# Optimization experiments

Measured on AMD Instinct MI355X. Metric: run time of the kernel, lower is better.

## Reference

```python
import jax, jax.numpy as jnp
import numpy as np

DIM = 1024
DIM_HEADS = 64  # number of heads in this module (per-head dim is 1, see source quirk)


def setup_inputs() -> dict:
    key = jax.random.key(0)
    k1, k2, k3 = jax.random.split(key, 3)
    x = jax.random.normal(k1, (1, 2048, DIM), dtype=jnp.float32)
    # torch Linear weight layout: [out_features, in_features]
    w_qkv = jax.random.normal(k2, (DIM_HEADS * 3, DIM), dtype=jnp.float32) * 0.02
    w_out = jax.random.normal(k3, (DIM, DIM_HEADS), dtype=jnp.float32) * 0.02
    return {"x": x, "w_qkv": w_qkv, "w_out": w_out}


def reference(x, w_qkv, w_out):
    b, n, _ = x.shape
    h = DIM_HEADS
    qkv = jnp.einsum('bnc,fc->bnf', x, w_qkv)          # [b, n, 3*h]
    q, k, v = jnp.split(qkv, 3, axis=-1)                # each [b, n, h]
    # rearrange 'b n (h d) -> b h n d' with h = DIM_HEADS => d = 1
    q = q.transpose(0, 2, 1)[..., None]                 # [b, h, n, 1]
    k = k.transpose(0, 2, 1)[..., None]
    v = v.transpose(0, 2, 1)[..., None]
    scale = 1.0 / jnp.sqrt(jnp.float32(h))              # source divides by sqrt(dim_heads)
    dots = jnp.einsum('bhid,bhjd->bhij', q, k) * scale  # [b, h, n, n]
    causal = jnp.tril(jnp.ones((n, n), dtype=bool))
    dots = jnp.where(causal, dots, -jnp.inf)
    attn = jax.nn.softmax(dots, axis=-1)
    out = jnp.einsum('bhij,bhjd->bhid', attn, v)        # [b, h, n, 1]
    out = out[..., 0].transpose(0, 2, 1)                # [b, n, h]
    return jnp.einsum('bnh,ch->bnc', out, w_out)        # [b, n, dim]
```

## Files before the change

kernel.cpp:

```cpp
#include <hip/hip_runtime.h>


#if __has_builtin(__builtin_amdgcn_exp2f)
#define EXP2F(x) __builtin_amdgcn_exp2f(x)
#else
#define EXP2F(x) exp2f(x)
#endif

#define LOG2E_DIV8 0.18033688011112042f

__global__ __launch_bounds__(256) void prep_kernel(const float* __restrict__ wqkv,
                                                   const float* __restrict__ wout,
                                                   float* __restrict__ wT,
                                                   float* __restrict__ wOutT) {
    const int b = blockIdx.x;
    if (b < 768) {
        int idx = b * 256 + threadIdx.x;
        int f = idx >> 10, k = idx & 1023;
        float val = wqkv[idx];
        if (f >= 64 && f < 128) val *= LOG2E_DIV8;
        wT[k * 192 + f] = val;
    } else {
        int idx = (b - 768) * 256 + threadIdx.x;
        int cc = idx >> 6, hh = idx & 63;
        wOutT[hh * 1024 + cc] = wout[idx];
    }
}

__global__ __launch_bounds__(256) void qkv_gemm(const float* __restrict__ x,
                                                const float* __restrict__ wT,
                                                float* __restrict__ pq) {
    __shared__ float xsT[32][64];
    __shared__ float wsld[32][64];
    const int t = threadIdx.x;
    const int b = blockIdx.x;
    const int ks = b & 7;
    const int nt = (b >> 3) % 3;
    const int mt = b / 24;
    const int i0 = mt * 64;
    const int cb = nt * 64;
    const int k0 = ks * 128;

    const int rf = t & 63;
    const int kq = t >> 6;
    const int tx = t & 15;
    const int ty = t >> 4;

    const float* xp = x + (size_t)(i0 + rf) * 1024 + k0 + kq * 8;
    const float* wp = wT + (size_t)(k0 + kq * 8) * 192 + cb + rf;

    float4 xa = *(const float4*)(xp);
    float4 xb = *(const float4*)(xp + 4);
    float wr[8];
#pragma unroll
    for (int j = 0; j < 8; ++j) wr[j] = wp[(size_t)j * 192];

    float acc[4][4] = {};

    for (int s = 0; s < 4; ++s) {
        __syncthreads();
        {
            const int kb = kq * 8;
            xsT[kb + 0][rf] = xa.x; xsT[kb + 1][rf] = xa.y;
            xsT[kb + 2][rf] = xa.z; xsT[kb + 3][rf] = xa.w;
            xsT[kb + 4][rf] = xb.x; xsT[kb + 5][rf] = xb.y;
            xsT[kb + 6][rf] = xb.z; xsT[kb + 7][rf] = xb.w;
#pragma unroll
            for (int j = 0; j < 8; ++j) wsld[kb + j][rf] = wr[j];
        }
        __syncthreads();
        if (s < 3) {
            const float* xp2 = xp + (s + 1) * 32;
            xa = *(const float4*)(xp2);
            xb = *(const float4*)(xp2 + 4);
            const float* wp2 = wp + (size_t)(s + 1) * 32 * 192;
#pragma unroll
            for (int j = 0; j < 8; ++j) wr[j] = wp2[(size_t)j * 192];
        }
#pragma unroll
        for (int k = 0; k < 32; ++k) {
            float4 a4 = *(const float4*)&xsT[k][ty * 4];
            float4 b4 = *(const float4*)&wsld[k][tx * 4];
            acc[0][0] = fmaf(a4.x, b4.x, acc[0][0]);
            acc[0][1] = fmaf(a4.x, b4.y, acc[0][1]);
            acc[0][2] = fmaf(a4.x, b4.z, acc[0][2]);
            acc[0][3] = fmaf(a4.x, b4.w, acc[0][3]);
            acc[1][0] = fmaf(a4.y, b4.x, acc[1][0]);
            acc[1][1] = fmaf(a4.y, b4.y, acc[1][1]);
            acc[1][2] = fmaf(a4.y, b4.z, acc[1][2]);
            acc[1][3] = fmaf(a4.y, b4.w, acc[1][3]);
            acc[2][0] = fmaf(a4.z, b4.x, acc[2][0]);
            acc[2][1] = fmaf(a4.z, b4.y, acc[2][1]);
            acc[2][2] = fmaf(a4.z, b4.z, acc[2][2]);
            acc[2][3] = fmaf(a4.z, b4.w, acc[2][3]);
            acc[3][0] = fmaf(a4.w, b4.x, acc[3][0]);
            acc[3][1] = fmaf(a4.w, b4.y, acc[3][1]);
            acc[3][2] = fmaf(a4.w, b4.z, acc[3][2]);
            acc[3][3] = fmaf(a4.w, b4.w, acc[3][3]);
        }
    }

    float* pbase = pq + (size_t)ks * 192 * 2048 + (size_t)cb * 2048 + i0;
#pragma unroll
    for (int cc = 0; cc < 4; ++cc) {
        float4 o = make_float4(acc[0][cc], acc[1][cc], acc[2][cc], acc[3][cc]);
        *(float4*)(pbase + (size_t)(tx * 4 + cc) * 2048 + ty * 4) = o;
    }
}

__global__ __launch_bounds__(256) void qkv_reduce(const float* __restrict__ pq,
                                                  float* __restrict__ qsv) {
    const int idx = blockIdx.x * 256 + threadIdx.x;
    const int f = idx >> 9;
    const int i = (idx & 511) * 4;
    const size_t S = (size_t)192 * 2048;
    const size_t o = (size_t)f * 2048 + i;
    float4 a0 = *(const float4*)(pq + o);
    float4 a1 = *(const float4*)(pq + S + o);
    float4 a2 = *(const float4*)(pq + 2 * S + o);
    float4 a3 = *(const float4*)(pq + 3 * S + o);
    float4 a4 = *(const float4*)(pq + 4 * S + o);
    float4 a5 = *(const float4*)(pq + 5 * S + o);
    float4 a6 = *(const float4*)(pq + 6 * S + o);
    float4 a7 = *(const float4*)(pq + 7 * S + o);
    float4 r = make_float4(((a0.x + a1.x) + (a2.x + a3.x)) + ((a4.x + a5.x) + (a6.x + a7.x)),
                           ((a0.y + a1.y) + (a2.y + a3.y)) + ((a4.y + a5.y) + (a6.y + a7.y)),
                           ((a0.z + a1.z) + (a2.z + a3.z)) + ((a4.z + a5.z) + (a6.z + a7.z)),
                           ((a0.w + a1.w) + (a2.w + a3.w)) + ((a4.w + a5.w) + (a6.w + a7.w)));
    const int which = f >> 6;
    const int h = f & 63;
    *(float4*)(qsv + (size_t)which * 131072 + (size_t)h * 2048 + i) = r;
}

__global__ __launch_bounds__(256) void attn_kernel(const float* __restrict__ qsv,
                                                   float* __restrict__ pn,
                                                   float* __restrict__ pd) {
    __shared__ float ssk[2048];
    __shared__ float svv[2048];
    const int t = threadIdx.x;
    const int h = blockIdx.x & 63;
    const int p = blockIdx.x >> 6;
    const int lane = t & 63;
    const int c = t >> 6;

    const int Alen = (p + 1) * 64;
    const int L    = (32 - p) * 64;
    const float* skp = qsv + 131072 + (size_t)h * 2048;
    const float* vp  = qsv + 262144 + (size_t)h * 2048;

    for (int idx = t * 4; idx < L; idx += 1024) {
        *(float4*)&ssk[idx] = *(const float4*)(skp + idx);
        *(float4*)&svv[idx] = *(const float4*)(vp + idx);
    }
    __syncthreads();

    const int i1 = Alen - 64 + lane;
    const int i2 = L - 64 + lane;
    const float qv1 = qsv[(size_t)h * 2048 + i1];
    const float qv2 = qsv[(size_t)h * 2048 + i2];

    float dA[4] = {0.f, 0.f, 0.f, 0.f}, nA[4] = {0.f, 0.f, 0.f, 0.f};
    float dB[4] = {0.f, 0.f, 0.f, 0.f}, nB[4] = {0.f, 0.f, 0.f, 0.f};

    const int gs = c * 528, ge = gs + 528;

    if (gs < Alen) {
        const int a1 = (ge < Alen) ? ge : Alen;
        const int d1 = Alen - 64;
        const int be = (a1 < d1) ? a1 : d1;
        for (int j = gs; j < be; j += 16) {
#pragma unroll
            for (int u = 0; u < 4; ++u) {
                float4 s = *(const float4*)&ssk[j + 4 * u];
                float4 v = *(const float4*)&svv[j + 4 * u];
                float e0 = EXP2F(qv1 * s.x), e1 = EXP2F(qv1 * s.y);
                float e2 = EXP2F(qv1 * s.z), e3 = EXP2F(qv1 * s.w);
                dA[0] += e0; nA[0] = fmaf(e0, v.x, nA[0]);
                dA[1] += e1; nA[1] = fmaf(e1, v.y, nA[1]);
                dA[2] += e2; nA[2] = fmaf(e2, v.z, nA[2]);
                dA[3] += e3; nA[3] = fmaf(e3, v.w, nA[3]);
            }
        }
        const int ms = (gs > d1) ? gs : d1;
        for (int j = ms; j < a1; j += 16) {
#pragma unroll
            for (int u = 0; u < 4; ++u) {
                float4 s = *(const float4*)&ssk[j + 4 * u];
                float4 v = *(const float4*)&svv[j + 4 * u];
                const int jb = j + 4 * u;
                float e0 = (jb     <= i1) ? EXP2F(qv1 * s.x) : 0.f;
                float e1 = (jb + 1 <= i1) ? EXP2F(qv1 * s.y) : 0.f;
                float e2 = (jb + 2 <= i1) ? EXP2F(qv1 * s.z) : 0.f;
                float e3 = (jb + 3 <= i1) ? EXP2F(qv1 * s.w) : 0.f;
                dA[0] += e0; nA[0] = fmaf(e0, v.x, nA[0]);
                dA[1] += e1; nA[1] = fmaf(e1, v.y, nA[1]);
                dA[2] += e2; nA[2] = fmaf(e2, v.z, nA[2]);
                dA[3] += e3; nA[3] = fmaf(e3, v.w, nA[3]);
            }
        }
    }

    if (ge > Alen) {
        const int b0 = ((gs > Alen) ? gs : Alen) - Alen;
        const int b1 = ge - Alen;
        const int d2 = L - 64;
        const int be = (b1 < d2) ? b1 : d2;
        for (int j = b0; j < be; j += 16) {
#pragma unroll
            for (int u = 0; u < 4; ++u) {
                float4 s = *(const float4*)&ssk[j + 4 * u];
                float4 v = *(const float4*)&svv[j + 4 * u];
                float e0 = EXP2F(qv2 * s.x), e1 = EXP2F(qv2 * s.y);
                float e2 = EXP2F(qv2 * s.z), e3 = EXP2F(qv2 * s.w);
                dB[0] += e0; nB[0] = fmaf(e0, v.x, nB[0]);
                dB[1] += e1; nB[1] = fmaf(e1, v.y, nB[1]);
                dB[2] += e2; nB[2] = fmaf(e2, v.z, nB[2]);
                dB[3] += e3; nB[3] = fmaf(e3, v.w, nB[3]);
            }
        }
        const int ms = (b0 > d2) ? b0 : d2;
        for (int j = ms; j < b1; j += 16) {
#pragma unroll
            for (int u = 0; u < 4; ++u) {
                float4 s = *(const float4*)&ssk[j + 4 * u];
                float4 v = *(const float4*)&svv[j + 4 * u];
                const int jb = j + 4 * u;
                float e0 = (jb     <= i2) ? EXP2F(qv2 * s.x) : 0.f;
                float e1 = (jb + 1 <= i2) ? EXP2F(qv2 * s.y) : 0.f;
                float e2 = (jb + 2 <= i2) ? EXP2F(qv2 * s.z) : 0.f;
                float e3 = (jb + 3 <= i2) ? EXP2F(qv2 * s.w) : 0.f;
                dB[0] += e0; nB[0] = fmaf(e0, v.x, nB[0]);
                dB[1] += e1; nB[1] = fmaf(e1, v.y, nB[1]);
                dB[2] += e2; nB[2] = fmaf(e2, v.z, nB[2]);
                dB[3] += e3; nB[3] = fmaf(e3, v.w, nB[3]);
            }
        }
    }

    const size_t base = ((size_t)c * 64 + h) * 2048;
    pn[base + i1] = (nA[0] + nA[1]) + (nA[2] + nA[3]);
    pd[base + i1] = (dA[0] + dA[1]) + (dA[2] + dA[3]);
    pn[base + i2] = (nB[0] + nB[1]) + (nB[2] + nB[3]);
    pd[base + i2] = (dB[0] + dB[1]) + (dB[2] + dB[3]);
}

__global__ __launch_bounds__(256) void proj_kernel(const float* __restrict__ pn,
                                                   const float* __restrict__ pd,
                                                   const float* __restrict__ wOutT,
                                                   float* __restrict__ out) {
    __shared__ float ast[64][8];
    const int t = threadIdx.x;
    const int i0 = (blockIdx.x >> 3) * 8;
    const int c0 = (blockIdx.x & 7) * 128;

    for (int s = t; s < 512; s += 256) {
        const int hh = s >> 3, ii = s & 7;
        const size_t o = (size_t)hh * 2048 + i0 + ii;
        float n = (pn[o] + pn[131072 + o]) + (pn[262144 + o] + pn[393216 + o]);
        float d = (pd[o] + pd[131072 + o]) + (pd[262144 + o] + pd[393216 + o]);
        ast[hh][ii] = n / d;
    }
    __syncthreads();

    const int rg = t >> 5;
    const int cg = t & 31;
    const float* wp = wOutT + c0 + cg * 4;
    float a0 = 0.f, a1 = 0.f, a2 = 0.f, a3 = 0.f;
#pragma unroll 8
    for (int hc = 0; hc < 64; ++hc) {
        float4 w4 = *(const float4*)(wp + (size_t)hc * 1024);
        float a = ast[hc][rg];
        a0 = fmaf(a, w4.x, a0);
        a1 = fmaf(a, w4.y, a1);
        a2 = fmaf(a, w4.z, a2);
        a3 = fmaf(a, w4.w, a3);
    }
    *(float4*)(out + (size_t)(i0 + rg) * 1024 + c0 + cg * 4) = make_float4(a0, a1, a2, a3);
}

extern "C" void kernel_launch(void* const* d_in, const int* in_sizes, int n_in,
                              void* d_out, int out_size, void* d_ws, size_t ws_size,
                              hipStream_t stream) {
    const float* x     = (const float*)d_in[0];
    const float* w_qkv = (const float*)d_in[1];
    const float* w_out = (const float*)d_in[2];
    float* out = (float*)d_out;

    float* ws    = (float*)d_ws;
    float* wT    = ws;
    float* wOutT = wT + 196608;
    float* qsv   = wOutT + 65536;
    float* scr   = qsv + 393216;
    float* pq    = scr;
    float* pn    = scr;
    float* pd    = scr + 524288;

    prep_kernel<<<dim3(1024), dim3(256), 0, stream>>>(w_qkv, w_out, wT, wOutT);
    qkv_gemm<<<dim3(768), dim3(256), 0, stream>>>(x, wT, pq);
    qkv_reduce<<<dim3(384), dim3(256), 0, stream>>>(pq, qsv);
    attn_kernel<<<dim3(1024), dim3(256), 0, stream>>>(qsv, pn, pd);
    proj_kernel<<<dim3(2048), dim3(256), 0, stream>>>(pn, pd, wOutT, out);
}
```

Before: 127.0 us.

## Retile QKV GEMM, widen attention blocks with in-block reduction, tile weight transpose

The weight-prep kernel now transposes through shared-memory tiles with vectorized reads instead of scattered per-element writes. The QKV GEMM uses 128-row tiles with a 16-way K split and 8x4 register blocking per thread, and the reduce kernel sums 16 partials. The attention kernel runs 512 threads, reduces its partial numerators and denominators in shared memory and writes normalized outputs directly. This lets the projection kernel read one array instead of combining four partials. More split-K partial traffic and higher register pressure are the trade-offs.

Result: faster. 122.6 us (-3.5%).

```diff
diff --git a/kernel.cpp b/kernel.cpp
--- a/kernel.cpp
+++ b/kernel.cpp
@@ -13,98 +13,134 @@
                                                    const float* __restrict__ wout,
                                                    float* __restrict__ wT,
                                                    float* __restrict__ wOutT) {
+    __shared__ float tile[64][65];
+    const int t = threadIdx.x;
     const int b = blockIdx.x;
-    if (b < 768) {
-        int idx = b * 256 + threadIdx.x;
-        int f = idx >> 10, k = idx & 1023;
-        float val = wqkv[idx];
-        if (f >= 64 && f < 128) val *= LOG2E_DIV8;
-        wT[k * 192 + f] = val;
+    const int r = t & 63;
+    const int g = t >> 6;
+    if (b < 48) {
+        const int f0 = (b % 3) * 64;
+        const int k0 = (b / 3) * 64;
+#pragma unroll
+        for (int j = 0; j < 4; ++j) {
+            float4 v = *(const float4*)(wqkv + (size_t)(f0 + r) * 1024 + k0 + g * 16 + j * 4);
+            tile[r][g * 16 + j * 4 + 0] = v.x;
+            tile[r][g * 16 + j * 4 + 1] = v.y;
+            tile[r][g * 16 + j * 4 + 2] = v.z;
+            tile[r][g * 16 + j * 4 + 3] = v.w;
+        }
+        __syncthreads();
+        const float sc = (f0 == 64) ? LOG2E_DIV8 : 1.0f;
+#pragma unroll
+        for (int j = 0; j < 16; ++j) {
+            const int k = k0 + g * 16 + j;
+            wT[(size_t)k * 192 + f0 + r] = tile[r][g * 16 + j] * sc;
+        }
     } else {
-        int idx = (b - 768) * 256 + threadIdx.x;
-        int cc = idx >> 6, hh = idx & 63;
-        wOutT[hh * 1024 + cc] = wout[idx];
+        const int c0 = (b - 48) * 64;
+#pragma unroll
+        for (int j = 0; j < 4; ++j) {
+            float4 v = *(const float4*)(wout + (size_t)(c0 + r) * 64 + g * 16 + j * 4);
+            tile[r][g * 16 + j * 4 + 0] = v.x;
+            tile[r][g * 16 + j * 4 + 1] = v.y;
+            tile[r][g * 16 + j * 4 + 2] = v.z;
+            tile[r][g * 16 + j * 4 + 3] = v.w;
+        }
+        __syncthreads();
+#pragma unroll
+        for (int j = 0; j < 16; ++j) {
+            const int h = g * 16 + j;
+            wOutT[(size_t)h * 1024 + c0 + r] = tile[r][h];
+        }
     }
 }
 
 __global__ __launch_bounds__(256) void qkv_gemm(const float* __restrict__ x,
                                                 const float* __restrict__ wT,
                                                 float* __restrict__ pq) {
-    __shared__ float xsT[32][64];
+    __shared__ float xsT[32][128];
     __shared__ float wsld[32][64];
     const int t = threadIdx.x;
     const int b = blockIdx.x;
-    const int ks = b & 7;
-    const int nt = (b >> 3) % 3;
-    const int mt = b / 24;
-    const int i0 = mt * 64;
+    const int ks = b & 15;
+    const int nt = (b >> 4) % 3;
+    const int mt = b / 48;
+    const int i0 = mt * 128;
     const int cb = nt * 64;
-    const int k0 = ks * 128;
-
-    const int rf = t & 63;
-    const int kq = t >> 6;
+    const int k0 = ks * 64;
+
+    const int xr = t & 127;
+    const int xq = t >> 7;
+    const int wf = t & 63;
+    const int wq = t >> 6;
     const int tx = t & 15;
     const int ty = t >> 4;
 
-    const float* xp = x + (size_t)(i0 + rf) * 1024 + k0 + kq * 8;
-    const float* wp = wT + (size_t)(k0 + kq * 8) * 192 + cb + rf;
-
-    float4 xa = *(const float4*)(xp);
-    float4 xb = *(const float4*)(xp + 4);
+    const float* xp = x + (size_t)(i0 + xr) * 1024 + k0 + xq * 16;
+    const float* wp = wT + (size_t)(k0 + wq * 8) * 192 + cb + wf;
+
+    float4 xa0 = *(const float4*)(xp);
+    float4 xa1 = *(const float4*)(xp + 4);
+    float4 xa2 = *(const float4*)(xp + 8);
+    float4 xa3 = *(const float4*)(xp + 12);
     float wr[8];
 #pragma unroll
     for (int j = 0; j < 8; ++j) wr[j] = wp[(size_t)j * 192];
 
-    float acc[4][4] = {};
-
-    for (int s = 0; s < 4; ++s) {
+    float acc[8][4] = {};
+
+    for (int s = 0; s < 2; ++s) {
         __syncthreads();
         {
-            const int kb = kq * 8;
-            xsT[kb + 0][rf] = xa.x; xsT[kb + 1][rf] = xa.y;
-            xsT[kb + 2][rf] = xa.z; xsT[kb + 3][rf] = xa.w;
-            xsT[kb + 4][rf] = xb.x; xsT[kb + 5][rf] = xb.y;
-            xsT[kb + 6][rf] = xb.z; xsT[kb + 7][rf] = xb.w;
-#pragma unroll
-            for (int j = 0; j < 8; ++j) wsld[kb + j][rf] = wr[j];
+            const int kb = xq * 16;
+            xsT[kb + 0][xr] = xa0.x; xsT[kb + 1][xr] = xa0.y;
+            xsT[kb + 2][xr] = xa0.z; xsT[kb + 3][xr] = xa0.w;
+            xsT[kb + 4][xr] = xa1.x; xsT[kb + 5][xr] = xa1.y;
+            xsT[kb + 6][xr] = xa1.z; xsT[kb + 7][xr] = xa1.w;
+            xsT[kb + 8][xr] = xa2.x; xsT[kb + 9][xr] = xa2.y;
+            xsT[kb + 10][xr] = xa2.z; xsT[kb + 11][xr] = xa2.w;
+            xsT[kb + 12][xr] = xa3.x; xsT[kb + 13][xr] = xa3.y;
+            xsT[kb + 14][xr] = xa3.z; xsT[kb + 15][xr] = xa3.w;
+            const int kw = wq * 8;
+#pragma unroll
+            for (int j = 0; j < 8; ++j) wsld[kw + j][wf] = wr[j];
         }
         __syncthreads();
-        if (s < 3) {
-            const float* xp2 = xp + (s + 1) * 32;
-            xa = *(const float4*)(xp2);
-            xb = *(const float4*)(xp2 + 4);
-            const float* wp2 = wp + (size_t)(s + 1) * 32 * 192;
+        if (s == 0) {
+            xa0 = *(const float4*)(xp + 32);
+            xa1 = *(const float4*)(xp + 36);
+            xa2 = *(const float4*)(xp + 40);
+            xa3 = *(const float4*)(xp + 44);
+            const float* wp2 = wp + (size_t)32 * 192;
 #pragma unroll
             for (int j = 0; j < 8; ++j) wr[j] = wp2[(size_t)j * 192];
         }
 #pragma unroll
         for (int k = 0; k < 32; ++k) {
-            float4 a4 = *(const float4*)&xsT[k][ty * 4];
+            float4 a0 = *(const float4*)&xsT[k][ty * 8];
+            float4 a1 = *(const float4*)&xsT[k][ty * 8 + 4];
             float4 b4 = *(const float4*)&wsld[k][tx * 4];
-            acc[0][0] = fmaf(a4.x, b4.x, acc[0][0]);
-            acc[0][1] = fmaf(a4.x, b4.y, acc[0][1]);
-            acc[0][2] = fmaf(a4.x, b4.z, acc[0][2]);
-            acc[0][3] = fmaf(a4.x, b4.w, acc[0][3]);
-            acc[1][0] = fmaf(a4.y, b4.x, acc[1][0]);
-            acc[1][1] = fmaf(a4.y, b4.y, acc[1][1]);
-            acc[1][2] = fmaf(a4.y, b4.z, acc[1][2]);
-            acc[1][3] = fmaf(a4.y, b4.w, acc[1][3]);
-            acc[2][0] = fmaf(a4.z, b4.x, acc[2][0]);
-            acc[2][1] = fmaf(a4.z, b4.y, acc[2][1]);
-            acc[2][2] = fmaf(a4.z, b4.z, acc[2][2]);
-            acc[2][3] = fmaf(a4.z, b4.w, acc[2][3]);
-            acc[3][0] = fmaf(a4.w, b4.x, acc[3][0]);
-            acc[3][1] = fmaf(a4.w, b4.y, acc[3][1]);
-            acc[3][2] = fmaf(a4.w, b4.z, acc[3][2]);
-            acc[3][3] = fmaf(a4.w, b4.w, acc[3][3]);
+#pragma unroll
+            for (int cc = 0; cc < 4; ++cc) {
+                const float bb = (cc == 0) ? b4.x : (cc == 1) ? b4.y : (cc == 2) ? b4.z : b4.w;
+                acc[0][cc] = fmaf(a0.x, bb, acc[0][cc]);
+                acc[1][cc] = fmaf(a0.y, bb, acc[1][cc]);
+                acc[2][cc] = fmaf(a0.z, bb, acc[2][cc]);
+                acc[3][cc] = fmaf(a0.w, bb, acc[3][cc]);
+                acc[4][cc] = fmaf(a1.x, bb, acc[4][cc]);
+                acc[5][cc] = fmaf(a1.y, bb, acc[5][cc]);
+                acc[6][cc] = fmaf(a1.z, bb, acc[6][cc]);
+                acc[7][cc] = fmaf(a1.w, bb, acc[7][cc]);
+            }
         }
     }
 
     float* pbase = pq + (size_t)ks * 192 * 2048 + (size_t)cb * 2048 + i0;
 #pragma unroll
     for (int cc = 0; cc < 4; ++cc) {
-        float4 o = make_float4(acc[0][cc], acc[1][cc], acc[2][cc], acc[3][cc]);
-        *(float4*)(pbase + (size_t)(tx * 4 + cc) * 2048 + ty * 4) = o;
+        float* dst = pbase + (size_t)(tx * 4 + cc) * 2048 + ty * 8;
+        *(float4*)(dst)     = make_float4(acc[0][cc], acc[1][cc], acc[2][cc], acc[3][cc]);
+        *(float4*)(dst + 4) = make_float4(acc[4][cc], acc[5][cc], acc[6][cc], acc[7][cc]);
     }
 }
 
@@ -115,28 +151,23 @@
     const int i = (idx & 511) * 4;
     const size_t S = (size_t)192 * 2048;
     const size_t o = (size_t)f * 2048 + i;
-    float4 a0 = *(const float4*)(pq + o);
-    float4 a1 = *(const float4*)(pq + S + o);
-    float4 a2 = *(const float4*)(pq + 2 * S + o);
-    float4 a3 = *(const float4*)(pq + 3 * S + o);
-    float4 a4 = *(const float4*)(pq + 4 * S + o);
-    float4 a5 = *(const float4*)(pq + 5 * S + o);
-    float4 a6 = *(const float4*)(pq + 6 * S + o);
-    float4 a7 = *(const float4*)(pq + 7 * S + o);
-    float4 r = make_float4(((a0.x + a1.x) + (a2.x + a3.x)) + ((a4.x + a5.x) + (a6.x + a7.x)),
-                           ((a0.y + a1.y) + (a2.y + a3.y)) + ((a4.y + a5.y) + (a6.y + a7.y)),
-                           ((a0.z + a1.z) + (a2.z + a3.z)) + ((a4.z + a5.z) + (a6.z + a7.z)),
-                           ((a0.w + a1.w) + (a2.w + a3.w)) + ((a4.w + a5.w) + (a6.w + a7.w)));
+    float sx = 0.f, sy = 0.f, sz = 0.f, sw = 0.f;
+#pragma unroll
+    for (int s = 0; s < 16; ++s) {
+        float4 a = *(const float4*)(pq + (size_t)s * S + o);
+        sx += a.x; sy += a.y; sz += a.z; sw += a.w;
+    }
     const int which = f >> 6;
     const int h = f & 63;
-    *(float4*)(qsv + (size_t)which * 131072 + (size_t)h * 2048 + i) = r;
-}
-
-__global__ __launch_bounds__(256) void attn_kernel(const float* __restrict__ qsv,
-                                                   float* __restrict__ pn,
-                                                   float* __restrict__ pd) {
+    *(float4*)(qsv + (size_t)which * 131072 + (size_t)h * 2048 + i) =
+        make_float4(sx, sy, sz, sw);
+}
+
+__global__ __launch_bounds__(512) void attn_kernel(const float* __restrict__ qsv,
+                                                   float* __restrict__ aws) {
     __shared__ float ssk[2048];
     __shared__ float svv[2048];
+    __shared__ float red[8][64][5];
     const int t = threadIdx.x;
     const int h = blockIdx.x & 63;
     const int p = blockIdx.x >> 6;
@@ -148,7 +179,7 @@
     const float* skp = qsv + 131072 + (size_t)h * 2048;
     const float* vp  = qsv + 262144 + (size_t)h * 2048;
 
-    for (int idx = t * 4; idx < L; idx += 1024) {
+    for (int idx = t * 4; idx < L; idx += 2048) {
         *(float4*)&ssk[idx] = *(const float4*)(skp + idx);
         *(float4*)&svv[idx] = *(const float4*)(vp + idx);
     }
@@ -162,15 +193,15 @@
     float dA[4] = {0.f, 0.f, 0.f, 0.f}, nA[4] = {0.f, 0.f, 0.f, 0.f};
     float dB[4] = {0.f, 0.f, 0.f, 0.f}, nB[4] = {0.f, 0.f, 0.f, 0.f};
 
-    const int gs = c * 528, ge = gs + 528;
+    const int gs = c * 264, ge = gs + 264;
 
     if (gs < Alen) {
         const int a1 = (ge < Alen) ? ge : Alen;
         const int d1 = Alen - 64;
         const int be = (a1 < d1) ? a1 : d1;
-        for (int j = gs; j < be; j += 16) {
-#pragma unroll
-            for (int u = 0; u < 4; ++u) {
+        for (int j = gs; j < be; j += 8) {
+#pragma unroll
+            for (int u = 0; u < 2; ++u) {
                 float4 s = *(const float4*)&ssk[j + 4 * u];
                 float4 v = *(const float4*)&svv[j + 4 * u];
                 float e0 = EXP2F(qv1 * s.x), e1 = EXP2F(qv1 * s.y);
@@ -182,9 +213,9 @@
             }
         }
         const int ms = (gs > d1) ? gs : d1;
-        for (int j = ms; j < a1; j += 16) {
-#pragma unroll
-            for (int u = 0; u < 4; ++u) {
+        for (int j = ms; j < a1; j += 8) {
+#pragma unroll
+            for (int u = 0; u < 2; ++u) {
                 float4 s = *(const float4*)&ssk[j + 4 * u];
                 float4 v = *(const float4*)&svv[j + 4 * u];
                 const int jb = j + 4 * u;
@@ -205,9 +236,9 @@
         const int b1 = ge - Alen;
         const int d2 = L - 64;
         const int be = (b1 < d2) ? b1 : d2;
-        for (int j = b0; j < be; j += 16) {
-#pragma unroll
-            for (int u = 0; u < 4; ++u) {
+        for (int j = b0; j < be; j += 8) {
+#pragma unroll
+            for (int u = 0; u < 2; ++u) {
                 float4 s = *(const float4*)&ssk[j + 4 * u];
                 float4 v = *(const float4*)&svv[j + 4 * u];
                 float e0 = EXP2F(qv2 * s.x), e1 = EXP2F(qv2 * s.y);
@@ -219,9 +250,9 @@
             }
         }
         const int ms = (b0 > d2) ? b0 : d2;
-        for (int j = ms; j < b1; j += 16) {
-#pragma unroll
-            for (int u = 0; u < 4; ++u) {
+        for (int j = ms; j < b1; j += 8) {
+#pragma unroll
+            for (int u = 0; u < 2; ++u) {
                 float4 s = *(const float4*)&ssk[j + 4 * u];
                 float4 v = *(const float4*)&svv[j + 4 * u];
                 const int jb = j + 4 * u;
@@ -237,15 +268,27 @@
         }
     }
 
-    const size_t base = ((size_t)c * 64 + h) * 2048;
-    pn[base + i1] = (nA[0] + nA[1]) + (nA[2] + nA[3]);
-    pd[base + i1] = (dA[0] + dA[1]) + (dA[2] + dA[3]);
-    pn[base + i2] = (nB[0] + nB[1]) + (nB[2] + nB[3]);
-    pd[base + i2] = (dB[0] + dB[1]) + (dB[2] + dB[3]);
-}
-
-__global__ __launch_bounds__(256) void proj_kernel(const float* __restrict__ pn,
-                                                   const float* __restrict__ pd,
+    red[c][lane][0] = (nA[0] + nA[1]) + (nA[2] + nA[3]);
+    red[c][lane][1] = (dA[0] + dA[1]) + (dA[2] + dA[3]);
+    red[c][lane][2] = (nB[0] + nB[1]) + (nB[2] + nB[3]);
+    red[c][lane][3] = (dB[0] + dB[1]) + (dB[2] + dB[3]);
+    __syncthreads();
+
+    if (t < 64) {
+        float n = 0.f, d = 0.f;
+#pragma unroll
+        for (int s = 0; s < 8; ++s) { n += red[s][t][0]; d += red[s][t][1]; }
+        aws[(size_t)h * 2048 + (Alen - 64 + t)] = n / d;
+    } else if (t < 128) {
+        const int l = t - 64;
+        float n = 0.f, d = 0.f;
+#pragma unroll
+        for (int s = 0; s < 8; ++s) { n += red[s][l][2]; d += red[s][l][3]; }
+        aws[(size_t)h * 2048 + (L - 64 + l)] = n / d;
+    }
+}
+
+__global__ __launch_bounds__(256) void proj_kernel(const float* __restrict__ aws,
                                                    const float* __restrict__ wOutT,
                                                    float* __restrict__ out) {
     __shared__ float ast[64][8];
@@ -255,10 +298,7 @@
 
     for (int s = t; s < 512; s += 256) {
         const int hh = s >> 3, ii = s & 7;
-        const size_t o = (size_t)hh * 2048 + i0 + ii;
-        float n = (pn[o] + pn[131072 + o]) + (pn[262144 + o] + pn[393216 + o]);
-        float d = (pd[o] + pd[131072 + o]) + (pd[262144 + o] + pd[393216 + o]);
-        ast[hh][ii] = n / d;
+        ast[hh][ii] = aws[(size_t)hh * 2048 + i0 + ii];
     }
     __syncthreads();
 
@@ -290,14 +330,12 @@
     float* wT    = ws;
     float* wOutT = wT + 196608;
     float* qsv   = wOutT + 65536;
-    float* scr   = qsv + 393216;
-    float* pq    = scr;
-    float* pn    = scr;
-    float* pd    = scr + 524288;
-
-    prep_kernel<<<dim3(1024), dim3(256), 0, stream>>>(w_qkv, w_out, wT, wOutT);
+    float* aws   = qsv + 393216;
+    float* pq    = aws + 131072;
+
+    prep_kernel<<<dim3(64), dim3(256), 0, stream>>>(w_qkv, w_out, wT, wOutT);
     qkv_gemm<<<dim3(768), dim3(256), 0, stream>>>(x, wT, pq);
     qkv_reduce<<<dim3(384), dim3(256), 0, stream>>>(pq, qsv);
-    attn_kernel<<<dim3(1024), dim3(256), 0, stream>>>(qsv, pn, pd);
-    proj_kernel<<<dim3(2048), dim3(256), 0, stream>>>(pn, pd, wOutT, out);
-}
+    attn_kernel<<<dim3(1024), dim3(512), 0, stream>>>(qsv, aws);
+    proj_kernel<<<dim3(2048), dim3(256), 0, stream>>>(aws, wOutT, out);
+}
```
